# Optimization experiments

Measured on AMD Instinct MI355X. Metric: run time of the kernel, lower is better.

Reference implementation:

```python
import jax, jax.numpy as jnp
import numpy as np

N_NODES = 170000
N_EDGES = 1200000
IN_FEATS = 128
N_HIDDEN = 256
N_CLASSES = 40
BN_EPS = 1e-5


def setup_inputs() -> dict:
    key = jax.random.key(0)
    ks = jax.random.split(key, 12)
    feat = jax.random.normal(ks[0], (N_NODES, IN_FEATS), dtype=jnp.float32)
    src = jax.random.randint(ks[1], (N_EDGES,), 0, N_NODES, dtype=jnp.int32)
    dst = jax.random.randint(ks[2], (N_EDGES,), 0, N_NODES, dtype=jnp.int32)
    # GraphConv weights (glorot-ish scale) and last-layer bias
    W0 = jax.random.normal(ks[3], (IN_FEATS, N_HIDDEN), dtype=jnp.float32) * (1.0 / np.sqrt(IN_FEATS))
    W1 = jax.random.normal(ks[4], (N_HIDDEN, N_HIDDEN), dtype=jnp.float32) * (1.0 / np.sqrt(N_HIDDEN))
    W2 = jax.random.normal(ks[5], (N_HIDDEN, N_CLASSES), dtype=jnp.float32) * (1.0 / np.sqrt(N_HIDDEN))
    b2 = jnp.zeros((N_CLASSES,), dtype=jnp.float32)
    # BatchNorm affine params for the two hidden layers
    g0 = jnp.ones((N_HIDDEN,), dtype=jnp.float32)
    beta0 = jnp.zeros((N_HIDDEN,), dtype=jnp.float32)
    g1 = jnp.ones((N_HIDDEN,), dtype=jnp.float32)
    beta1 = jnp.zeros((N_HIDDEN,), dtype=jnp.float32)
    return {"feat": feat, "src": src, "dst": dst, "W0": W0, "W1": W1, "W2": W2,
            "b2": b2, "g0": g0, "beta0": beta0, "g1": g1, "beta1": beta1}


def _batchnorm(h, gamma, beta):
    mean = jnp.mean(h, axis=0)
    var = jnp.mean((h - mean) ** 2, axis=0)  # biased var, torch training-mode norm
    return (h - mean) * jax.lax.rsqrt(var + BN_EPS) * gamma + beta


def reference(feat, src, dst, W0, W1, W2, b2, g0, beta0, g1, beta1):
    n = feat.shape[0]
    ones_e = jnp.ones(src.shape, dtype=feat.dtype)
    deg_out = jnp.clip(jax.ops.segment_sum(ones_e, src, num_segments=n), 1.0)
    deg_in = jnp.clip(jax.ops.segment_sum(ones_e, dst, num_segments=n), 1.0)
    norm_src = deg_out ** -0.5  # [N]
    norm_dst = deg_in ** -0.5   # [N]

    def conv(h, W, bias=None):
        # GraphConv 'both': D_out^{-1/2} message, sum-aggregate, D_in^{-1/2}
        h = h @ W                              # project first (out <= in)
        msg = h[src] * norm_src[src][:, None]  # [E, out]
        agg = jax.ops.segment_sum(msg, dst, num_segments=n) * norm_dst[:, None]
        if bias is not None:
            agg = agg + bias
        return agg

    # dropout layers are identity in this deterministic (eval-style) reference
    h = conv(feat, W0)
    h = jax.nn.relu(_batchnorm(h, g0, beta0))
    h = conv(h, W1)
    h = jax.nn.relu(_batchnorm(h, g1, beta1))
    h = conv(h, W2, b2)
    return h
```

## Files before the change

kernel.cpp:

```cpp
#include <hip/hip_runtime.h>

#define NN 170000
#define NE 1200000
#define F_IN 128
#define F_HID 256
#define F_OUT 40
#define BN_EPS 1e-5f
#define SCAN_B ((NN + 255) / 256)
#define GB_TILES ((NN + 127) / 128)
#define STAT_ROWS (2 * GB_TILES)
#define STAT_CHUNK 32
#define STAT_NCH ((STAT_ROWS + STAT_CHUNK - 1) / STAT_CHUNK)

typedef __attribute__((ext_vector_type(8))) short short8;
typedef __attribute__((ext_vector_type(4))) float f32x4;
typedef __attribute__((ext_vector_type(4))) unsigned short us4;
typedef __attribute__((ext_vector_type(4))) unsigned int u32x4;

__device__ __forceinline__ float b2f(unsigned short u) {
    union { unsigned x; float f; } c; c.x = ((unsigned)u) << 16; return c.f;
}
__device__ __forceinline__ unsigned short f2b(float f) {
    union { float f; unsigned x; } c; c.f = f;
    unsigned r = (c.x + 0x7FFFu + ((c.x >> 16) & 1u)) >> 16;
    return (unsigned short)r;
}
__device__ __forceinline__ unsigned bn2(unsigned u, float a0, float b0, float a1, float b1) {
    float lo = b2f((unsigned short)(u & 0xffffu));
    float hi = b2f((unsigned short)(u >> 16));
    lo = fmaxf(lo * a0 + b0, 0.0f);
    hi = fmaxf(hi * a1 + b1, 0.0f);
    return (unsigned)f2b(lo) | ((unsigned)f2b(hi) << 16);
}

__global__ void count_kernel(const int* __restrict__ src, const int* __restrict__ dst,
                             int* __restrict__ cnt_src, int* __restrict__ cnt_dst, int E) {
    int e = blockIdx.x * blockDim.x + threadIdx.x;
    if (e < E) {
        atomicAdd(&cnt_src[src[e]], 1);
        atomicAdd(&cnt_dst[dst[e]], 1);
    }
}

__global__ void norm_kernel(const int* __restrict__ cnt_src, const int* __restrict__ cnt_dst,
                            float* __restrict__ norm_src, float* __restrict__ norm_dst, int N) {
    int i = blockIdx.x * blockDim.x + threadIdx.x;
    if (i < N) {
        norm_src[i] = rsqrtf((float)max(cnt_src[i], 1));
        norm_dst[i] = rsqrtf((float)max(cnt_dst[i], 1));
    }
}

__global__ void scan_block_kernel(const int* __restrict__ cnt, int* __restrict__ local,
                                  int* __restrict__ partials, int N) {
    __shared__ int s[256];
    int t = threadIdx.x;
    int idx = blockIdx.x * 256 + t;
    int v = (idx < N) ? cnt[idx] : 0;
    s[t] = v;
    __syncthreads();
    #pragma unroll
    for (int off = 1; off < 256; off <<= 1) {
        int x = (t >= off) ? s[t - off] : 0;
        __syncthreads();
        s[t] += x;
        __syncthreads();
    }
    if (idx < N) local[idx] = s[t] - v;
    if (t == 255) partials[blockIdx.x] = s[t];
}

__global__ void scan_partials_kernel(int* __restrict__ partials, int B) {
    __shared__ int s[1024];
    int t = threadIdx.x;
    int v = (t < B) ? partials[t] : 0;
    s[t] = v;
    __syncthreads();
    #pragma unroll
    for (int off = 1; off < 1024; off <<= 1) {
        int x = (t >= off) ? s[t - off] : 0;
        __syncthreads();
        s[t] += x;
        __syncthreads();
    }
    if (t < B) partials[t] = s[t] - v;
}

__global__ void scan_add_kernel(const int* __restrict__ local, const int* __restrict__ partials,
                                int* __restrict__ row_ptr, int N) {
    int idx = blockIdx.x * blockDim.x + threadIdx.x;
    if (idx < N) row_ptr[idx] = local[idx] + partials[idx >> 8];
    if (idx == 0) row_ptr[N] = NE;
}

__global__ void fill_kernel(const int* __restrict__ src, const int* __restrict__ dst,
                            const int* __restrict__ row_ptr, int* __restrict__ fill,
                            int* __restrict__ csr_src, int E) {
    int e = blockIdx.x * blockDim.x + threadIdx.x;
    if (e < E) {
        int d = dst[e];
        int pos = row_ptr[d] + atomicAdd(&fill[d], 1);
        csr_src[pos] = src[e];
    }
}

__global__ void cast_feat_kernel(const float* __restrict__ feat, const float* __restrict__ norm_src,
                                 unsigned short* __restrict__ featb) {
    unsigned idx = blockIdx.x * blockDim.x + threadIdx.x;
    if (idx >= (unsigned)NN * (F_IN / 4)) return;
    float ns = norm_src[idx / (F_IN / 4)];
    f32x4 v = __builtin_nontemporal_load((const f32x4*)(feat + (size_t)idx * 4));
    us4 o; o.x = f2b(v.x * ns); o.y = f2b(v.y * ns); o.z = f2b(v.z * ns); o.w = f2b(v.w * ns);
    *(us4*)(featb + (size_t)idx * 4) = o;
}

template<int F, bool FUSE>
__global__ void gather_sum_kernel(const unsigned short* __restrict__ h, const int* __restrict__ row_ptr,
                                  const int* __restrict__ csr_src,
                                  const float* __restrict__ bna, const float* __restrict__ bnb,
                                  const float* __restrict__ norm_src,
                                  unsigned short* __restrict__ out, int N) {
    constexpr int TPN = F / 4;
    unsigned idx = blockIdx.x * blockDim.x + threadIdx.x;
    if (idx >= (unsigned)N * TPN) return;
    unsigned node = idx / TPN;
    unsigned g = idx % TPN;
    f32x4 ca = {0.f, 0.f, 0.f, 0.f}, cb = {0.f, 0.f, 0.f, 0.f};
    if (FUSE) {
        ca = *(const f32x4*)(bna + g * 4);
        cb = *(const f32x4*)(bnb + g * 4);
    }
    int beg = row_ptr[node], end = row_ptr[node + 1];
    float ax0 = 0.f, ay0 = 0.f, az0 = 0.f, aw0 = 0.f;
    float ax1 = 0.f, ay1 = 0.f, az1 = 0.f, aw1 = 0.f;
    int e = beg;
    for (; e + 2 <= end; e += 2) {
        int s0 = csr_src[e], s1 = csr_src[e + 1];
        const us4 v0 = *(const us4*)(h + (size_t)s0 * F + g * 4);
        const us4 v1 = *(const us4*)(h + (size_t)s1 * F + g * 4);
        if (FUSE) {
            float n0 = norm_src[s0], n1 = norm_src[s1];
            ax0 += fmaxf(fmaf(b2f(v0.x), ca.x, cb.x), 0.f) * n0;
            ay0 += fmaxf(fmaf(b2f(v0.y), ca.y, cb.y), 0.f) * n0;
            az0 += fmaxf(fmaf(b2f(v0.z), ca.z, cb.z), 0.f) * n0;
            aw0 += fmaxf(fmaf(b2f(v0.w), ca.w, cb.w), 0.f) * n0;
            ax1 += fmaxf(fmaf(b2f(v1.x), ca.x, cb.x), 0.f) * n1;
            ay1 += fmaxf(fmaf(b2f(v1.y), ca.y, cb.y), 0.f) * n1;
            az1 += fmaxf(fmaf(b2f(v1.z), ca.z, cb.z), 0.f) * n1;
            aw1 += fmaxf(fmaf(b2f(v1.w), ca.w, cb.w), 0.f) * n1;
        } else {
            ax0 += b2f(v0.x); ay0 += b2f(v0.y); az0 += b2f(v0.z); aw0 += b2f(v0.w);
            ax1 += b2f(v1.x); ay1 += b2f(v1.y); az1 += b2f(v1.z); aw1 += b2f(v1.w);
        }
    }
    if (e < end) {
        int s0 = csr_src[e];
        const us4 v0 = *(const us4*)(h + (size_t)s0 * F + g * 4);
        if (FUSE) {
            float n0 = norm_src[s0];
            ax0 += fmaxf(fmaf(b2f(v0.x), ca.x, cb.x), 0.f) * n0;
            ay0 += fmaxf(fmaf(b2f(v0.y), ca.y, cb.y), 0.f) * n0;
            az0 += fmaxf(fmaf(b2f(v0.z), ca.z, cb.z), 0.f) * n0;
            aw0 += fmaxf(fmaf(b2f(v0.w), ca.w, cb.w), 0.f) * n0;
        } else {
            ax0 += b2f(v0.x); ay0 += b2f(v0.y); az0 += b2f(v0.z); aw0 += b2f(v0.w);
        }
    }
    us4 o;
    o.x = f2b(ax0 + ax1); o.y = f2b(ay0 + ay1); o.z = f2b(az0 + az1); o.w = f2b(aw0 + aw1);
    __builtin_nontemporal_store(o, (us4*)(out + (size_t)node * F + g * 4));
}

__global__ void gather_final_kernel(const float* __restrict__ h, const int* __restrict__ row_ptr,
                                    const int* __restrict__ csr_src,
                                    const float* __restrict__ norm_dst, const float* __restrict__ bias,
                                    float* __restrict__ out, int N) {
    constexpr int TPN = F_OUT / 4;
    unsigned idx = blockIdx.x * blockDim.x + threadIdx.x;
    if (idx >= (unsigned)N * TPN) return;
    unsigned node = idx / TPN;
    unsigned g = idx % TPN;
    int beg = row_ptr[node], end = row_ptr[node + 1];
    float ax0 = 0.f, ay0 = 0.f, az0 = 0.f, aw0 = 0.f;
    float ax1 = 0.f, ay1 = 0.f, az1 = 0.f, aw1 = 0.f;
    int e = beg;
    for (; e + 2 <= end; e += 2) {
        int s0 = csr_src[e], s1 = csr_src[e + 1];
        const f32x4 v0 = *(const f32x4*)(h + (size_t)s0 * F_OUT + g * 4);
        const f32x4 v1 = *(const f32x4*)(h + (size_t)s1 * F_OUT + g * 4);
        ax0 += v0.x; ay0 += v0.y; az0 += v0.z; aw0 += v0.w;
        ax1 += v1.x; ay1 += v1.y; az1 += v1.z; aw1 += v1.w;
    }
    if (e < end) {
        int s0 = csr_src[e];
        const f32x4 v0 = *(const f32x4*)(h + (size_t)s0 * F_OUT + g * 4);
        ax0 += v0.x; ay0 += v0.y; az0 += v0.z; aw0 += v0.w;
    }
    float nd = norm_dst[node];
    const f32x4 b = *(const f32x4*)(bias + g * 4);
    f32x4 r;
    r.x = (ax0 + ax1) * nd + b.x; r.y = (ay0 + ay1) * nd + b.y;
    r.z = (az0 + az1) * nd + b.z; r.w = (aw0 + aw1) * nd + b.w;
    __builtin_nontemporal_store(r, (f32x4*)(out + (size_t)node * F_OUT + g * 4));
}

template<int K, int M, int MP>
__global__ void wt_kernel(const float* __restrict__ W, unsigned short* __restrict__ Wt) {
    int idx = blockIdx.x * blockDim.x + threadIdx.x;
    if (idx >= MP * K) return;
    int m = idx / K, k = idx % K;
    float v = (m < M) ? W[(size_t)k * M + m] : 0.0f;
    Wt[idx] = f2b(v);
}

__global__ void stat_reduce_kernel(const float* __restrict__ part, float* __restrict__ red) {
    int c = threadIdx.x;
    int ch = blockIdx.x;
    int r0 = ch * STAT_CHUNK;
    int r1 = min(r0 + STAT_CHUNK, STAT_ROWS);
    float s = 0.f;
    for (int r = r0; r < r1; r++) s += part[(size_t)r * 512 + c];
    red[ch * 512 + c] = s;
}

__global__ void bn_finalize2_kernel(const float* __restrict__ red,
                                    const float* __restrict__ gamma, const float* __restrict__ beta,
                                    float* __restrict__ a, float* __restrict__ b) {
    int c = threadIdx.x;
    float sum = 0.f, sumsq = 0.f;
    for (int ch = 0; ch < STAT_NCH; ch++) {
        sum   += red[ch * 512 + c];
        sumsq += red[ch * 512 + 256 + c];
    }
    float invN = 1.0f / (float)NN;
    float mean = sum * invN;
    float var = sumsq * invN - mean * mean;
    float inv = rsqrtf(var + BN_EPS);
    float ac = inv * gamma[c];
    a[c] = ac;
    b[c] = beta[c] - mean * ac;
}

template<int K, int BN_T, int WM_T, int WN_T, int WAVES_N, bool SCALE, bool BF16OUT, int M_OUT,
         bool STATS, bool APPLYBN>
__global__ __launch_bounds__(256, 3) void mfma_gemm(const unsigned short* __restrict__ A,
                                                    const unsigned short* __restrict__ Wt,
                                                    const float* __restrict__ rowscale,
                                                    void* __restrict__ C,
                                                    const float* __restrict__ bna,
                                                    const float* __restrict__ bnb,
                                                    float* __restrict__ opart, int N) {
    constexpr int BM = 128;
    constexpr int WAVES_M = 4 / WAVES_N;
    const int lane = threadIdx.x & 63;
    const int wave = threadIdx.x >> 6;
    const int wr = wave / WAVES_N, wc = wave % WAVES_N;
    const int quad = lane >> 4, l15 = lane & 15;
    const int r0 = blockIdx.y * BM;
    const int c0 = blockIdx.x * BN_T;
    const int wmb = wr * WM_T * 16;
    const int wnb = wc * WN_T * 16;

    const unsigned short* aptr[WM_T];
    #pragma unroll
    for (int i = 0; i < WM_T; i++) {
        int gr = r0 + wmb + i * 16 + l15;
        if (gr > N - 1) gr = N - 1;
        aptr[i] = A + (size_t)gr * K + quad * 8;
    }
    const unsigned short* bptr[WN_T];
    #pragma unroll
    for (int j = 0; j < WN_T; j++)
        bptr[j] = Wt + (size_t)(c0 + wnb + j * 16 + l15) * K + quad * 8;

    f32x4 acc[WM_T][WN_T] = {};

    #pragma unroll
    for (int kk = 0; kk < K; kk += 32) {
        short8 af[WM_T], bf[WN_T];
        f32x4 a0 = {0,0,0,0}, a1 = {0,0,0,0}, s0 = {0,0,0,0}, s1 = {0,0,0,0};
        if (APPLYBN) {
            int kb = kk + quad * 8;
            a0 = *(const f32x4*)(bna + kb);
            a1 = *(const f32x4*)(bna + kb + 4);
            s0 = *(const f32x4*)(bnb + kb);
            s1 = *(const f32x4*)(bnb + kb + 4);
        }
        #pragma unroll
        for (int i = 0; i < WM_T; i++) {
            if (APPLYBN) {
                u32x4 u = *(const u32x4*)(aptr[i] + kk);
                u.x = bn2(u.x, a0.x, s0.x, a0.y, s0.y);
                u.y = bn2(u.y, a0.z, s0.z, a0.w, s0.w);
                u.z = bn2(u.z, a1.x, s1.x, a1.y, s1.y);
                u.w = bn2(u.w, a1.z, s1.z, a1.w, s1.w);
                af[i] = *(short8*)&u;
            } else {
                af[i] = *(const short8*)(aptr[i] + kk);
            }
        }
        #pragma unroll
        for (int j = 0; j < WN_T; j++)
            bf[j] = *(const short8*)(bptr[j] + kk);
        #pragma unroll
        for (int i = 0; i < WM_T; i++)
            #pragma unroll
            for (int j = 0; j < WN_T; j++)
                acc[i][j] = __builtin_amdgcn_mfma_f32_16x16x32_bf16(af[i], bf[j], acc[i][j], 0, 0, 0);
    }

    float s[WN_T] = {}, ss[WN_T] = {};
    #pragma unroll
    for (int i = 0; i < WM_T; i++) {
        #pragma unroll
        for (int r = 0; r < 4; r++) {
            int row = r0 + wmb + i * 16 + quad * 4 + r;
            if (row >= N) continue;
            float scale = SCALE ? rowscale[row] : 1.0f;
            #pragma unroll
            for (int j = 0; j < WN_T; j++) {
                float v = acc[i][j][r] * scale;
                if (STATS) { s[j] += v; ss[j] += v * v; }
                int col = c0 + wnb + j * 16 + l15;
                if (col < M_OUT) {
                    if (BF16OUT) ((unsigned short*)C)[(size_t)row * M_OUT + col] = f2b(v);
                    else         ((float*)C)[(size_t)row * M_OUT + col] = v;
                }
            }
        }
    }
    if (STATS) {
        #pragma unroll
        for (int j = 0; j < WN_T; j++) {
            float t = s[j], t2 = ss[j];
            t  += __shfl_xor(t, 16);  t  += __shfl_xor(t, 32);
            t2 += __shfl_xor(t2, 16); t2 += __shfl_xor(t2, 32);
            if (quad == 0) {
                int col = c0 + wnb + j * 16 + l15;
                size_t prow = (size_t)(blockIdx.y * WAVES_M + wr) * 512;
                opart[prow + col] = t;
                opart[prow + 256 + col] = t2;
            }
        }
    }
}

extern "C" void kernel_launch(void* const* d_in, const int* in_sizes, int n_in,
                              void* d_out, int out_size, void* d_ws, size_t ws_size,
                              hipStream_t stream) {
    const float* feat  = (const float*)d_in[0];
    const int*   src   = (const int*)d_in[1];
    const int*   dst   = (const int*)d_in[2];
    const float* W0    = (const float*)d_in[3];
    const float* W1    = (const float*)d_in[4];
    const float* W2    = (const float*)d_in[5];
    const float* b2    = (const float*)d_in[6];
    const float* g0    = (const float*)d_in[7];
    const float* beta0 = (const float*)d_in[8];
    const float* g1    = (const float*)d_in[9];
    const float* beta1 = (const float*)d_in[10];
    float* out = (float*)d_out;

    const int N = NN, E = NE;

    char* ws = (char*)d_ws;
    auto alloc_b = [&](size_t bytes) {
        void* p = (void*)ws;
        ws += ((bytes + 255) / 256) * 256;
        return p;
    };
    float* norm_src = (float*)alloc_b((size_t)N * 4);
    float* norm_dst = (float*)alloc_b((size_t)N * 4);
    int*   row_ptr  = (int*)alloc_b((size_t)(N + 1) * 4);
    int*   csr_src  = (int*)alloc_b((size_t)E * 4);
    float* bnpart   = (float*)alloc_b((size_t)STAT_ROWS * 512 * 4);
    float* bnred    = (float*)alloc_b((size_t)STAT_NCH * 512 * 4);
    float* bn_a0    = (float*)alloc_b(256 * 4);
    float* bn_b0    = (float*)alloc_b(256 * 4);
    float* bn_a1    = (float*)alloc_b(256 * 4);
    float* bn_b1    = (float*)alloc_b(256 * 4);
    unsigned short* Wt0 = (unsigned short*)alloc_b((size_t)256 * 128 * 2);
    unsigned short* Wt1 = (unsigned short*)alloc_b((size_t)256 * 256 * 2);
    unsigned short* Wt2 = (unsigned short*)alloc_b((size_t)64 * 256 * 2);
    void* B1 = alloc_b((size_t)N * 512);
    void* B2 = alloc_b((size_t)N * 512);
    unsigned short* featb = (unsigned short*)alloc_b((size_t)N * F_IN * 2);

    unsigned short* B1b = (unsigned short*)B1;
    unsigned short* B2b = (unsigned short*)B2;
    float*          B1f = (float*)B1;

    int* cnt_src  = (int*)B1;
    int* cnt_dst  = cnt_src + N;
    int* fill     = cnt_dst + N;
    int* local    = fill + N;
    int* partials = local + N;

    hipMemsetAsync(cnt_src, 0, ((size_t)4 * N + 1024) * 4, stream);
    count_kernel<<<(E + 255) / 256, 256, 0, stream>>>(src, dst, cnt_src, cnt_dst, E);
    norm_kernel<<<(N + 255) / 256, 256, 0, stream>>>(cnt_src, cnt_dst, norm_src, norm_dst, N);
    scan_block_kernel<<<SCAN_B, 256, 0, stream>>>(cnt_dst, local, partials, N);
    scan_partials_kernel<<<1, 1024, 0, stream>>>(partials, SCAN_B);
    scan_add_kernel<<<(N + 255) / 256, 256, 0, stream>>>(local, partials, row_ptr, N);
    fill_kernel<<<(E + 255) / 256, 256, 0, stream>>>(src, dst, row_ptr, fill, csr_src, E);
    wt_kernel<128, 256, 256><<<(256 * 128 + 255) / 256, 256, 0, stream>>>(W0, Wt0);
    wt_kernel<256, 256, 256><<<(256 * 256 + 255) / 256, 256, 0, stream>>>(W1, Wt1);
    wt_kernel<256, 40, 64><<<(64 * 256 + 255) / 256, 256, 0, stream>>>(W2, Wt2);
    cast_feat_kernel<<<((unsigned)N * (F_IN / 4) + 255) / 256, 256, 0, stream>>>(feat, norm_src, featb);

    const int GB = GB_TILES;

    {
        unsigned total = (unsigned)N * (F_IN / 4);
        gather_sum_kernel<F_IN, false><<<(total + 255) / 256, 256, 0, stream>>>(
            featb, row_ptr, csr_src, nullptr, nullptr, nullptr, B1b, N);
    }
    mfma_gemm<128, 128, 4, 4, 2, true, true, 256, true, false><<<dim3(2, GB), 256, 0, stream>>>(
        B1b, Wt0, norm_dst, B2, nullptr, nullptr, bnpart, N);
    stat_reduce_kernel<<<STAT_NCH, 512, 0, stream>>>(bnpart, bnred);
    bn_finalize2_kernel<<<1, 256, 0, stream>>>(bnred, g0, beta0, bn_a0, bn_b0);

    {
        unsigned total = (unsigned)N * (F_HID / 4);
        gather_sum_kernel<F_HID, true><<<(total + 255) / 256, 256, 0, stream>>>(
            B2b, row_ptr, csr_src, bn_a0, bn_b0, norm_src, B1b, N);
    }
    mfma_gemm<256, 128, 4, 4, 2, true, true, 256, true, false><<<dim3(2, GB), 256, 0, stream>>>(
        B1b, Wt1, norm_dst, B2, nullptr, nullptr, bnpart, N);
    stat_reduce_kernel<<<STAT_NCH, 512, 0, stream>>>(bnpart, bnred);
    bn_finalize2_kernel<<<1, 256, 0, stream>>>(bnred, g1, beta1, bn_a1, bn_b1);

    mfma_gemm<256, 64, 2, 4, 1, true, false, 40, false, true><<<dim3(1, GB), 256, 0, stream>>>(
        B2b, Wt2, norm_src, B1, bn_a1, bn_b1, nullptr, N);
    {
        unsigned total = (unsigned)N * (F_OUT / 4);
        gather_final_kernel<<<(total + 255) / 256, 256, 0, stream>>>(
            B1f, row_ptr, csr_src, norm_dst, b2, out, N);
    }
}
```

Baseline: 799.8 us.

## Fuse neighbor gather into MFMA GEMM via LDS tile for all layers

```diff
diff --git a/kernel.cpp b/kernel.cpp
--- a/kernel.cpp
+++ b/kernel.cpp
@@ -7,8 +7,8 @@
 #define F_OUT 40
 #define BN_EPS 1e-5f
 #define SCAN_B ((NN + 255) / 256)
-#define GB_TILES ((NN + 127) / 128)
-#define STAT_ROWS (2 * GB_TILES)
+#define GB64 ((NN + 63) / 64)
+#define STAT_ROWS GB64
 #define STAT_CHUNK 32
 #define STAT_NCH ((STAT_ROWS + STAT_CHUNK - 1) / STAT_CHUNK)
 
@@ -25,12 +25,23 @@
     unsigned r = (c.x + 0x7FFFu + ((c.x >> 16) & 1u)) >> 16;
     return (unsigned short)r;
 }
-__device__ __forceinline__ unsigned bn2(unsigned u, float a0, float b0, float a1, float b1) {
-    float lo = b2f((unsigned short)(u & 0xffffu));
-    float hi = b2f((unsigned short)(u >> 16));
-    lo = fmaxf(lo * a0 + b0, 0.0f);
-    hi = fmaxf(hi * a1 + b1, 0.0f);
-    return (unsigned)f2b(lo) | ((unsigned)f2b(hi) << 16);
+
+__device__ __forceinline__ void agg_sum(const u32x4& v, float (&aa)[8]) {
+    aa[0] += b2f((unsigned short)(v.x & 0xffffu)); aa[1] += b2f((unsigned short)(v.x >> 16));
+    aa[2] += b2f((unsigned short)(v.y & 0xffffu)); aa[3] += b2f((unsigned short)(v.y >> 16));
+    aa[4] += b2f((unsigned short)(v.z & 0xffffu)); aa[5] += b2f((unsigned short)(v.z >> 16));
+    aa[6] += b2f((unsigned short)(v.w & 0xffffu)); aa[7] += b2f((unsigned short)(v.w >> 16));
+}
+__device__ __forceinline__ void agg_fuse(const u32x4& v, float ns,
+        const f32x4& ca0, const f32x4& ca1, const f32x4& cb0, const f32x4& cb1, float (&aa)[8]) {
+    aa[0] += fmaxf(fmaf(b2f((unsigned short)(v.x & 0xffffu)), ca0.x, cb0.x), 0.f) * ns;
+    aa[1] += fmaxf(fmaf(b2f((unsigned short)(v.x >> 16)),     ca0.y, cb0.y), 0.f) * ns;
+    aa[2] += fmaxf(fmaf(b2f((unsigned short)(v.y & 0xffffu)), ca0.z, cb0.z), 0.f) * ns;
+    aa[3] += fmaxf(fmaf(b2f((unsigned short)(v.y >> 16)),     ca0.w, cb0.w), 0.f) * ns;
+    aa[4] += fmaxf(fmaf(b2f((unsigned short)(v.z & 0xffffu)), ca1.x, cb1.x), 0.f) * ns;
+    aa[5] += fmaxf(fmaf(b2f((unsigned short)(v.z >> 16)),     ca1.y, cb1.y), 0.f) * ns;
+    aa[6] += fmaxf(fmaf(b2f((unsigned short)(v.w & 0xffffu)), ca1.z, cb1.z), 0.f) * ns;
+    aa[7] += fmaxf(fmaf(b2f((unsigned short)(v.w >> 16)),     ca1.w, cb1.w), 0.f) * ns;
 }
 
 __global__ void count_kernel(const int* __restrict__ src, const int* __restrict__ dst,
@@ -114,96 +125,6 @@
     *(us4*)(featb + (size_t)idx * 4) = o;
 }
 
-template<int F, bool FUSE>
-__global__ void gather_sum_kernel(const unsigned short* __restrict__ h, const int* __restrict__ row_ptr,
-                                  const int* __restrict__ csr_src,
-                                  const float* __restrict__ bna, const float* __restrict__ bnb,
-                                  const float* __restrict__ norm_src,
-                                  unsigned short* __restrict__ out, int N) {
-    constexpr int TPN = F / 4;
-    unsigned idx = blockIdx.x * blockDim.x + threadIdx.x;
-    if (idx >= (unsigned)N * TPN) return;
-    unsigned node = idx / TPN;
-    unsigned g = idx % TPN;
-    f32x4 ca = {0.f, 0.f, 0.f, 0.f}, cb = {0.f, 0.f, 0.f, 0.f};
-    if (FUSE) {
-        ca = *(const f32x4*)(bna + g * 4);
-        cb = *(const f32x4*)(bnb + g * 4);
-    }
-    int beg = row_ptr[node], end = row_ptr[node + 1];
-    float ax0 = 0.f, ay0 = 0.f, az0 = 0.f, aw0 = 0.f;
-    float ax1 = 0.f, ay1 = 0.f, az1 = 0.f, aw1 = 0.f;
-    int e = beg;
-    for (; e + 2 <= end; e += 2) {
-        int s0 = csr_src[e], s1 = csr_src[e + 1];
-        const us4 v0 = *(const us4*)(h + (size_t)s0 * F + g * 4);
-        const us4 v1 = *(const us4*)(h + (size_t)s1 * F + g * 4);
-        if (FUSE) {
-            float n0 = norm_src[s0], n1 = norm_src[s1];
-            ax0 += fmaxf(fmaf(b2f(v0.x), ca.x, cb.x), 0.f) * n0;
-            ay0 += fmaxf(fmaf(b2f(v0.y), ca.y, cb.y), 0.f) * n0;
-            az0 += fmaxf(fmaf(b2f(v0.z), ca.z, cb.z), 0.f) * n0;
-            aw0 += fmaxf(fmaf(b2f(v0.w), ca.w, cb.w), 0.f) * n0;
-            ax1 += fmaxf(fmaf(b2f(v1.x), ca.x, cb.x), 0.f) * n1;
-            ay1 += fmaxf(fmaf(b2f(v1.y), ca.y, cb.y), 0.f) * n1;
-            az1 += fmaxf(fmaf(b2f(v1.z), ca.z, cb.z), 0.f) * n1;
-            aw1 += fmaxf(fmaf(b2f(v1.w), ca.w, cb.w), 0.f) * n1;
-        } else {
-            ax0 += b2f(v0.x); ay0 += b2f(v0.y); az0 += b2f(v0.z); aw0 += b2f(v0.w);
-            ax1 += b2f(v1.x); ay1 += b2f(v1.y); az1 += b2f(v1.z); aw1 += b2f(v1.w);
-        }
-    }
-    if (e < end) {
-        int s0 = csr_src[e];
-        const us4 v0 = *(const us4*)(h + (size_t)s0 * F + g * 4);
-        if (FUSE) {
-            float n0 = norm_src[s0];
-            ax0 += fmaxf(fmaf(b2f(v0.x), ca.x, cb.x), 0.f) * n0;
-            ay0 += fmaxf(fmaf(b2f(v0.y), ca.y, cb.y), 0.f) * n0;
-            az0 += fmaxf(fmaf(b2f(v0.z), ca.z, cb.z), 0.f) * n0;
-            aw0 += fmaxf(fmaf(b2f(v0.w), ca.w, cb.w), 0.f) * n0;
-        } else {
-            ax0 += b2f(v0.x); ay0 += b2f(v0.y); az0 += b2f(v0.z); aw0 += b2f(v0.w);
-        }
-    }
-    us4 o;
-    o.x = f2b(ax0 + ax1); o.y = f2b(ay0 + ay1); o.z = f2b(az0 + az1); o.w = f2b(aw0 + aw1);
-    __builtin_nontemporal_store(o, (us4*)(out + (size_t)node * F + g * 4));
-}
-
-__global__ void gather_final_kernel(const float* __restrict__ h, const int* __restrict__ row_ptr,
-                                    const int* __restrict__ csr_src,
-                                    const float* __restrict__ norm_dst, const float* __restrict__ bias,
-                                    float* __restrict__ out, int N) {
-    constexpr int TPN = F_OUT / 4;
-    unsigned idx = blockIdx.x * blockDim.x + threadIdx.x;
-    if (idx >= (unsigned)N * TPN) return;
-    unsigned node = idx / TPN;
-    unsigned g = idx % TPN;
-    int beg = row_ptr[node], end = row_ptr[node + 1];
-    float ax0 = 0.f, ay0 = 0.f, az0 = 0.f, aw0 = 0.f;
-    float ax1 = 0.f, ay1 = 0.f, az1 = 0.f, aw1 = 0.f;
-    int e = beg;
-    for (; e + 2 <= end; e += 2) {
-        int s0 = csr_src[e], s1 = csr_src[e + 1];
-        const f32x4 v0 = *(const f32x4*)(h + (size_t)s0 * F_OUT + g * 4);
-        const f32x4 v1 = *(const f32x4*)(h + (size_t)s1 * F_OUT + g * 4);
-        ax0 += v0.x; ay0 += v0.y; az0 += v0.z; aw0 += v0.w;
-        ax1 += v1.x; ay1 += v1.y; az1 += v1.z; aw1 += v1.w;
-    }
-    if (e < end) {
-        int s0 = csr_src[e];
-        const f32x4 v0 = *(const f32x4*)(h + (size_t)s0 * F_OUT + g * 4);
-        ax0 += v0.x; ay0 += v0.y; az0 += v0.z; aw0 += v0.w;
-    }
-    float nd = norm_dst[node];
-    const f32x4 b = *(const f32x4*)(bias + g * 4);
-    f32x4 r;
-    r.x = (ax0 + ax1) * nd + b.x; r.y = (ay0 + ay1) * nd + b.y;
-    r.z = (az0 + az1) * nd + b.z; r.w = (aw0 + aw1) * nd + b.w;
-    __builtin_nontemporal_store(r, (f32x4*)(out + (size_t)node * F_OUT + g * 4));
-}
-
 template<int K, int M, int MP>
 __global__ void wt_kernel(const float* __restrict__ W, unsigned short* __restrict__ Wt) {
     int idx = blockIdx.x * blockDim.x + threadIdx.x;
@@ -241,63 +162,90 @@
     b[c] = beta[c] - mean * ac;
 }
 
-template<int K, int BN_T, int WM_T, int WN_T, int WAVES_N, bool SCALE, bool BF16OUT, int M_OUT,
-         bool STATS, bool APPLYBN>
-__global__ __launch_bounds__(256, 3) void mfma_gemm(const unsigned short* __restrict__ A,
-                                                    const unsigned short* __restrict__ Wt,
-                                                    const float* __restrict__ rowscale,
-                                                    void* __restrict__ C,
-                                                    const float* __restrict__ bna,
-                                                    const float* __restrict__ bnb,
-                                                    float* __restrict__ opart, int N) {
-    constexpr int BM = 128;
+template<int F, int WM_T, int WN_T, int WAVES_N, bool FUSE, bool LAST>
+__global__ __launch_bounds__(256) void fused_gather_gemm(
+        const unsigned short* __restrict__ h,
+        const int* __restrict__ row_ptr, const int* __restrict__ csr_src,
+        const float* __restrict__ bna, const float* __restrict__ bnb,
+        const unsigned short* __restrict__ Wt,
+        const float* __restrict__ norm_src, const float* __restrict__ norm_dst,
+        const float* __restrict__ bias,
+        void* __restrict__ C, float* __restrict__ opart, int N) {
+    constexpr int BM = 64;
+    constexpr int LPN = F / 8;
+    constexpr int NPW = 64 / LPN;
     constexpr int WAVES_M = 4 / WAVES_N;
+    __shared__ unsigned short As[BM * F];
+
     const int lane = threadIdx.x & 63;
     const int wave = threadIdx.x >> 6;
+    const int r0 = blockIdx.x * BM;
+
+    {
+        const int sub = lane / LPN;
+        const int cl = lane % LPN;
+        f32x4 ca0 = {0,0,0,0}, ca1 = {0,0,0,0}, cb0 = {0,0,0,0}, cb1 = {0,0,0,0};
+        if (FUSE) {
+            ca0 = *(const f32x4*)(bna + cl * 8);
+            ca1 = *(const f32x4*)(bna + cl * 8 + 4);
+            cb0 = *(const f32x4*)(bnb + cl * 8);
+            cb1 = *(const f32x4*)(bnb + cl * 8 + 4);
+        }
+        #pragma unroll
+        for (int g = 0; g < 16 / NPW; g++) {
+            int nl = wave * 16 + g * NPW + sub;
+            int node = r0 + nl;
+            float aa[8] = {0.f, 0.f, 0.f, 0.f, 0.f, 0.f, 0.f, 0.f};
+            int beg = 0, end = 0;
+            if (node < N) { beg = row_ptr[node]; end = row_ptr[node + 1]; }
+            int e = beg;
+            for (; e + 2 <= end; e += 2) {
+                int s0 = csr_src[e], s1 = csr_src[e + 1];
+                u32x4 v0 = *(const u32x4*)(h + (size_t)s0 * F + cl * 8);
+                u32x4 v1 = *(const u32x4*)(h + (size_t)s1 * F + cl * 8);
+                if (FUSE) {
+                    agg_fuse(v0, norm_src[s0], ca0, ca1, cb0, cb1, aa);
+                    agg_fuse(v1, norm_src[s1], ca0, ca1, cb0, cb1, aa);
+                } else {
+                    agg_sum(v0, aa); agg_sum(v1, aa);
+                }
+            }
+            if (e < end) {
+                int s0 = csr_src[e];
+                u32x4 v0 = *(const u32x4*)(h + (size_t)s0 * F + cl * 8);
+                if (FUSE) agg_fuse(v0, norm_src[s0], ca0, ca1, cb0, cb1, aa);
+                else      agg_sum(v0, aa);
+            }
+            u32x4 d;
+            d.x = (unsigned)f2b(aa[0]) | ((unsigned)f2b(aa[1]) << 16);
+            d.y = (unsigned)f2b(aa[2]) | ((unsigned)f2b(aa[3]) << 16);
+            d.z = (unsigned)f2b(aa[4]) | ((unsigned)f2b(aa[5]) << 16);
+            d.w = (unsigned)f2b(aa[6]) | ((unsigned)f2b(aa[7]) << 16);
+            unsigned off = ((unsigned)(nl * (F * 2) + cl * 16)) ^ (((unsigned)nl & 7u) << 4);
+            *(u32x4*)((char*)As + off) = d;
+        }
+    }
+    __syncthreads();
+
+    const int quad = lane >> 4, l15 = lane & 15;
     const int wr = wave / WAVES_N, wc = wave % WAVES_N;
-    const int quad = lane >> 4, l15 = lane & 15;
-    const int r0 = blockIdx.y * BM;
-    const int c0 = blockIdx.x * BN_T;
     const int wmb = wr * WM_T * 16;
     const int wnb = wc * WN_T * 16;
 
-    const unsigned short* aptr[WM_T];
-    #pragma unroll
-    for (int i = 0; i < WM_T; i++) {
-        int gr = r0 + wmb + i * 16 + l15;
-        if (gr > N - 1) gr = N - 1;
-        aptr[i] = A + (size_t)gr * K + quad * 8;
-    }
     const unsigned short* bptr[WN_T];
     #pragma unroll
     for (int j = 0; j < WN_T; j++)
-        bptr[j] = Wt + (size_t)(c0 + wnb + j * 16 + l15) * K + quad * 8;
+        bptr[j] = Wt + (size_t)(wnb + j * 16 + l15) * F + quad * 8;
 
     f32x4 acc[WM_T][WN_T] = {};
-
-    #pragma unroll
-    for (int kk = 0; kk < K; kk += 32) {
+    #pragma unroll
+    for (int kk = 0; kk < F; kk += 32) {
         short8 af[WM_T], bf[WN_T];
-        f32x4 a0 = {0,0,0,0}, a1 = {0,0,0,0}, s0 = {0,0,0,0}, s1 = {0,0,0,0};
-        if (APPLYBN) {
-            int kb = kk + quad * 8;
-            a0 = *(const f32x4*)(bna + kb);
-            a1 = *(const f32x4*)(bna + kb + 4);
-            s0 = *(const f32x4*)(bnb + kb);
-            s1 = *(const f32x4*)(bnb + kb + 4);
-        }
         #pragma unroll
         for (int i = 0; i < WM_T; i++) {
-            if (APPLYBN) {
-                u32x4 u = *(const u32x4*)(aptr[i] + kk);
-                u.x = bn2(u.x, a0.x, s0.x, a0.y, s0.y);
-                u.y = bn2(u.y, a0.z, s0.z, a0.w, s0.w);
-                u.z = bn2(u.z, a1.x, s1.x, a1.y, s1.y);
-                u.w = bn2(u.w, a1.z, s1.z, a1.w, s1.w);
-                af[i] = *(short8*)&u;
-            } else {
-                af[i] = *(const short8*)(aptr[i] + kk);
-            }
+            int row = wmb + i * 16 + l15;
+            unsigned off = ((unsigned)(row * (F * 2) + (kk + quad * 8) * 2)) ^ (((unsigned)row & 7u) << 4);
+            af[i] = *(const short8*)((const char*)As + off);
         }
         #pragma unroll
         for (int j = 0; j < WN_T; j++)
@@ -316,28 +264,30 @@
         for (int r = 0; r < 4; r++) {
             int row = r0 + wmb + i * 16 + quad * 4 + r;
             if (row >= N) continue;
-            float scale = SCALE ? rowscale[row] : 1.0f;
+            float nd = norm_dst[row];
             #pragma unroll
             for (int j = 0; j < WN_T; j++) {
-                float v = acc[i][j][r] * scale;
-                if (STATS) { s[j] += v; ss[j] += v * v; }
-                int col = c0 + wnb + j * 16 + l15;
-                if (col < M_OUT) {
-                    if (BF16OUT) ((unsigned short*)C)[(size_t)row * M_OUT + col] = f2b(v);
-                    else         ((float*)C)[(size_t)row * M_OUT + col] = v;
+                float v = acc[i][j][r] * nd;
+                int col = wnb + j * 16 + l15;
+                if (LAST) {
+                    if (col < F_OUT)
+                        ((float*)C)[(size_t)row * F_OUT + col] = v + bias[col];
+                } else {
+                    s[j] += v; ss[j] += v * v;
+                    ((unsigned short*)C)[(size_t)row * F_HID + col] = f2b(v);
                 }
             }
         }
     }
-    if (STATS) {
+    if (!LAST) {
         #pragma unroll
         for (int j = 0; j < WN_T; j++) {
             float t = s[j], t2 = ss[j];
             t  += __shfl_xor(t, 16);  t  += __shfl_xor(t, 32);
             t2 += __shfl_xor(t2, 16); t2 += __shfl_xor(t2, 32);
             if (quad == 0) {
-                int col = c0 + wnb + j * 16 + l15;
-                size_t prow = (size_t)(blockIdx.y * WAVES_M + wr) * 512;
+                int col = wnb + j * 16 + l15;
+                size_t prow = (size_t)(blockIdx.x * WAVES_M + wr) * 512;
                 opart[prow + col] = t;
                 opart[prow + 256 + col] = t2;
             }
@@ -388,7 +338,6 @@
 
     unsigned short* B1b = (unsigned short*)B1;
     unsigned short* B2b = (unsigned short*)B2;
-    float*          B1f = (float*)B1;
 
     int* cnt_src  = (int*)B1;
     int* cnt_dst  = cnt_src + N;
@@ -408,33 +357,16 @@
     wt_kernel<256, 40, 64><<<(64 * 256 + 255) / 256, 256, 0, stream>>>(W2, Wt2);
     cast_feat_kernel<<<((unsigned)N * (F_IN / 4) + 255) / 256, 256, 0, stream>>>(feat, norm_src, featb);
 
-    const int GB = GB_TILES;
-
-    {
-        unsigned total = (unsigned)N * (F_IN / 4);
-        gather_sum_kernel<F_IN, false><<<(total + 255) / 256, 256, 0, stream>>>(
-            featb, row_ptr, csr_src, nullptr, nullptr, nullptr, B1b, N);
-    }
-    mfma_gemm<128, 128, 4, 4, 2, true, true, 256, true, false><<<dim3(2, GB), 256, 0, stream>>>(
-        B1b, Wt0, norm_dst, B2, nullptr, nullptr, bnpart, N);
+    fused_gather_gemm<128, 4, 4, 4, false, false><<<GB64, 256, 0, stream>>>(
+        featb, row_ptr, csr_src, nullptr, nullptr, Wt0, nullptr, norm_dst, nullptr, B1, bnpart, N);
     stat_reduce_kernel<<<STAT_NCH, 512, 0, stream>>>(bnpart, bnred);
     bn_finalize2_kernel<<<1, 256, 0, stream>>>(bnred, g0, beta0, bn_a0, bn_b0);
 
-    {
-        unsigned total = (unsigned)N * (F_HID / 4);
-        gather_sum_kernel<F_HID, true><<<(total + 255) / 256, 256, 0, stream>>>(
-            B2b, row_ptr, csr_src, bn_a0, bn_b0, norm_src, B1b, N);
-    }
-    mfma_gemm<256, 128, 4, 4, 2, true, true, 256, true, false><<<dim3(2, GB), 256, 0, stream>>>(
-        B1b, Wt1, norm_dst, B2, nullptr, nullptr, bnpart, N);
+    fused_gather_gemm<256, 4, 4, 4, true, false><<<GB64, 256, 0, stream>>>(
+        B1b, row_ptr, csr_src, bn_a0, bn_b0, Wt1, norm_src, norm_dst, nullptr, B2, bnpart, N);
     stat_reduce_kernel<<<STAT_NCH, 512, 0, stream>>>(bnpart, bnred);
     bn_finalize2_kernel<<<1, 256, 0, stream>>>(bnred, g1, beta1, bn_a1, bn_b1);
 
-    mfma_gemm<256, 64, 2, 4, 1, true, false, 40, false, true><<<dim3(1, GB), 256, 0, stream>>>(
-        B2b, Wt2, norm_src, B1, bn_a1, bn_b1, nullptr, N);
-    {
-        unsigned total = (unsigned)N * (F_OUT / 4);
-        gather_final_kernel<<<(total + 255) / 256, 256, 0, stream>>>(
-            B1f, row_ptr, csr_src, norm_dst, b2, out, N);
-    }
-}
+    fused_gather_gemm<256, 1, 3, 1, true, true><<<GB64, 256, 0, stream>>>(
+        B2b, row_ptr, csr_src, bn_a1, bn_b1, Wt2, norm_src, norm_dst, b2, out, nullptr, N);
+}
```

Result: slower. 819.9 us (+2.5%).
